# Kernel optimization log

Measured on AMD Instinct MI355X. Metric: run time of the kernel, lower is better.

## Reference

```python
import jax, jax.numpy as jnp
import numpy as np

B, N, D, H = 4, 1024, 1024, 16
HD = D // H  # 64
EPS = 1e-5


def rotate_half(t):
    # unflatten last dim to (..., HD//2, 2), swap-and-negate, flatten back
    t2 = t.reshape(t.shape[:-1] + (HD // 2, 2))
    x1, x2 = t2[..., 0], t2[..., 1]
    return jnp.stack((-x2, x1), axis=-1).reshape(t.shape)


def setup_inputs() -> dict:
    key = jax.random.key(0)
    ks = jax.random.split(key, 12)
    s = 0.02
    return {
        "x": jax.random.normal(ks[0], (B, N, D), jnp.float32),
        "encoding": jax.random.uniform(ks[1], (2, B, 1, N, HD), jnp.float32),
        "Wqkv_w": jax.random.normal(ks[2], (3 * D, D), jnp.float32) * s,
        "Wqkv_b": jnp.zeros((3 * D,), jnp.float32),
        "out_w": jax.random.normal(ks[3], (D, D), jnp.float32) * s,
        "out_b": jnp.zeros((D,), jnp.float32),
        "ffn1_w": jax.random.normal(ks[4], (2 * D, 2 * D), jnp.float32) * s,
        "ffn1_b": jnp.zeros((2 * D,), jnp.float32),
        "ln_g": jnp.ones((2 * D,), jnp.float32),
        "ln_b": jnp.zeros((2 * D,), jnp.float32),
        "ffn2_w": jax.random.normal(ks[5], (D, 2 * D), jnp.float32) * s,
        "ffn2_b": jnp.zeros((D,), jnp.float32),
    }


def reference(x, encoding, Wqkv_w, Wqkv_b, out_w, out_b,
              ffn1_w, ffn1_b, ln_g, ln_b, ffn2_w, ffn2_b):
    b, n, d = x.shape
    # fused QKV projection: [B,N,3D] -> [B,H,N,HD,3]
    qkv = x @ Wqkv_w.T + Wqkv_b
    qkv = qkv.reshape(b, n, H, HD, 3).transpose(0, 2, 1, 3, 4)
    q, k, v = qkv[..., 0], qkv[..., 1], qkv[..., 2]
    # cached rotary embedding: t*cos + rotate_half(t)*sin
    q = q * encoding[0] + rotate_half(q) * encoding[1]
    k = k * encoding[0] + rotate_half(k) * encoding[1]
    # scaled dot-product attention (mask is None in this path)
    scale = HD ** -0.5
    sim = jnp.einsum('bhid,bhjd->bhij', q, k) * scale
    attn = jax.nn.softmax(sim, axis=-1)
    ctx = jnp.einsum('bhij,bhjd->bhid', attn, v)
    ctx = ctx.transpose(0, 2, 1, 3).reshape(b, n, d)
    message = ctx @ out_w.T + out_b
    # FFN on concat([x, message]) with interposed LayerNorm + GELU (exact)
    h = jnp.concatenate([x, message], axis=-1) @ ffn1_w.T + ffn1_b
    mu = h.mean(-1, keepdims=True)
    var = ((h - mu) ** 2).mean(-1, keepdims=True)
    h = (h - mu) * jax.lax.rsqrt(var + EPS) * ln_g + ln_b
    h = jax.nn.gelu(h, approximate=False)
    return x + h @ ffn2_w.T + ffn2_b
```

## Files before the change

### kernel.cpp

```cpp
#include <hip/hip_runtime.h>
#include <hip/hip_bf16.h>
#include <math.h>

#define B_ 4
#define N_ 1024
#define D_ 1024
#define H_ 16
#define HD_ 64
#define M_ (B_*N_)

typedef __hip_bfloat16 bf16;
using floatx4 = __attribute__((ext_vector_type(4))) float;
using shortx8 = __attribute__((ext_vector_type(8))) short;

__device__ __forceinline__ float to_f(bf16 v) { return __bfloat162float(v); }
__device__ __forceinline__ float s2f(short v) {
    unsigned u = ((unsigned)(unsigned short)v) << 16;
    return __builtin_bit_cast(float, u);
}
__device__ __forceinline__ unsigned short bf_bits(float x) {
    bf16 h = __float2bfloat16(x);
    return *reinterpret_cast<unsigned short*>(&h);
}

#define GLOBAL_AS __attribute__((address_space(1)))
#define LDS_AS    __attribute__((address_space(3)))
__device__ __forceinline__ void load_lds16(const void* g, void* l) {
    __builtin_amdgcn_global_load_lds((const GLOBAL_AS unsigned int*)g,
                                     (LDS_AS unsigned int*)l, 16, 0, 0);
}

__device__ __forceinline__ void storec(float* p, float v) { *p = v; }
__device__ __forceinline__ void storec(bf16*  p, float v) { *p = __float2bfloat16(v); }

template<typename TC, bool RESID, bool SPLIT, int BN>
__global__ __launch_bounds__(256)
void mgemm(const bf16* __restrict__ A, int lda,
           const bf16* __restrict__ A2, int lda2, int K1,
           const bf16* __restrict__ W, int ldw,
           const float* __restrict__ bias,
           const float* __restrict__ resid, int ldr,
           TC* __restrict__ C, int ldc,
           int M, int N, int K)
{
    constexpr int NT  = BN / 32;
    constexpr int ASZ = 128 * 32;
    constexpr int BSZ = BN * 32;
    __shared__ short lds[2 * (ASZ + BSZ)];

    int t = threadIdx.x;
    int lane = t & 63, quad = lane >> 4, l15 = lane & 15;
    int wave = t >> 6, wm = wave & 1, wn = wave >> 1;

    int gx = gridDim.x;
    int bid = blockIdx.y * gx + blockIdx.x;
    int seg = bid / (8 * gx);
    int rem = bid - seg * 8 * gx;
    int bx = rem >> 3;
    int by = seg * 8 + (rem & 7);
    int row0 = by * 128, col0 = bx * BN;

    const short* Ag  = (const short*)A;
    const short* A2g = (const short*)A2;
    const short* Wg  = (const short*)W;

    auto stage = [&](int buf, int k0) {
        short* As = lds + buf * (ASZ + BSZ);
        short* Bs = As + ASZ;
        #pragma unroll
        for (int pass = 0; pass < 2; ++pass) {
            int idx = pass * 256 + t;
            int r = idx >> 2, c8 = (idx & 3) << 3;
            int wub = (pass * 256 + (t & 192)) * 8;
            const short* asrc;
            if (SPLIT && k0 >= K1)
                asrc = A2g + (size_t)(row0 + r) * lda2 + (k0 - K1) + c8;
            else
                asrc = Ag + (size_t)(row0 + r) * lda + k0 + c8;
            load_lds16(asrc, &As[wub]);
        }
        #pragma unroll
        for (int pass = 0; pass < BN / 64; ++pass) {
            int idx = pass * 256 + t;
            int r = idx >> 2, c8 = (idx & 3) << 3;
            int wub = (pass * 256 + (t & 192)) * 8;
            load_lds16(Wg + (size_t)(col0 + r) * ldw + k0 + c8, &Bs[wub]);
        }
    };

    floatx4 acc[4][NT];
    #pragma unroll
    for (int mt = 0; mt < 4; ++mt)
        #pragma unroll
        for (int nt = 0; nt < NT; ++nt)
            acc[mt][nt] = (floatx4){0.f, 0.f, 0.f, 0.f};

    stage(0, 0);
    int buf = 0;
    for (int k0 = 0; k0 < K; k0 += 32, buf ^= 1) {
        __syncthreads();
        const short* As = lds + buf * (ASZ + BSZ);
        const short* Bs = As + ASZ;
        shortx8 af[4], bfv[NT];
        #pragma unroll
        for (int mt = 0; mt < 4; ++mt)
            af[mt] = *(const shortx8*)&As[(wm * 64 + mt * 16 + l15) * 32 + quad * 8];
        #pragma unroll
        for (int nt = 0; nt < NT; ++nt)
            bfv[nt] = *(const shortx8*)&Bs[(wn * (BN / 2) + nt * 16 + l15) * 32 + quad * 8];
        if (k0 + 32 < K) stage(buf ^ 1, k0 + 32);
        #pragma unroll
        for (int mt = 0; mt < 4; ++mt)
            #pragma unroll
            for (int nt = 0; nt < NT; ++nt)
                acc[mt][nt] = __builtin_amdgcn_mfma_f32_16x16x32_bf16(
                    af[mt], bfv[nt], acc[mt][nt], 0, 0, 0);
    }

    #pragma unroll
    for (int mt = 0; mt < 4; ++mt) {
        #pragma unroll
        for (int nt = 0; nt < NT; ++nt) {
            int col = col0 + wn * (BN / 2) + nt * 16 + l15;
            float bv = bias[col];
            #pragma unroll
            for (int r = 0; r < 4; ++r) {
                int row = row0 + wm * 64 + mt * 16 + quad * 4 + r;
                float v = acc[mt][nt][r] + bv;
                if (RESID) v += resid[(size_t)row * ldr + col];
                storec(&C[(size_t)row * ldc + col], v);
            }
        }
    }
}

__global__ void f2b_all(const float* __restrict__ s0, bf16* __restrict__ d0,
                        const float* __restrict__ s1, bf16* __restrict__ d1,
                        const float* __restrict__ s2, bf16* __restrict__ d2,
                        const float* __restrict__ s3, bf16* __restrict__ d3,
                        const float* __restrict__ s4, bf16* __restrict__ d4)
{
    int blk = blockIdx.x;
    const float* s; bf16* d; int base;
    if      (blk < 4096)  { s = s0; d = d0; base = blk; }
    else if (blk < 7168)  { s = s1; d = d1; base = blk - 4096; }
    else if (blk < 8192)  { s = s2; d = d2; base = blk - 7168; }
    else if (blk < 12288) { s = s3; d = d3; base = blk - 8192; }
    else                  { s = s4; d = d4; base = blk - 12288; }
    int i = base * 1024 + threadIdx.x * 4;
    float4 v = *(const float4*)&s[i];
    d[i + 0] = __float2bfloat16(v.x);
    d[i + 1] = __float2bfloat16(v.y);
    d[i + 2] = __float2bfloat16(v.z);
    d[i + 3] = __float2bfloat16(v.w);
}

#define RS 196
__global__ __launch_bounds__(256)
void rope_all(const bf16* __restrict__ qkv, const float* __restrict__ enc,
              bf16* __restrict__ q, bf16* __restrict__ k, bf16* __restrict__ vt)
{
    __shared__ short raw[64 * RS];
    int n0 = blockIdx.x * 64, h = blockIdx.y, b = blockIdx.z;
    int t = threadIdx.x;
    const short* qg = (const short*)qkv;

    {
        int row = t >> 2, off = (t & 3) * 48;
        const short* src = qg + ((size_t)(b * N_ + n0 + row)) * 3072 + h * 192 + off;
        uint4 u[3];
        u[0] = ((const uint4*)src)[0];
        u[1] = ((const uint4*)src)[1];
        u[2] = ((const uint4*)src)[2];
        uint4 u2[3];
        u2[0] = ((const uint4*)src)[3];
        u2[1] = ((const uint4*)src)[4];
        u2[2] = ((const uint4*)src)[5];
        uint2* dst = (uint2*)&raw[row * RS + off];
        const uint2* p = (const uint2*)u;
        #pragma unroll
        for (int i = 0; i < 6; ++i) dst[i] = p[i];
        const uint2* p2 = (const uint2*)u2;
        #pragma unroll
        for (int i = 0; i < 6; ++i) dst[6 + i] = p2[i];
    }
    __syncthreads();

    size_t bh = (size_t)(b * H_ + h);
    {
        int d = t & 63, g0 = t >> 6;
        int dp = d ^ 1;
        float sgn = (d & 1) ? 1.0f : -1.0f;
        #pragma unroll
        for (int i = 0; i < 16; ++i) {
            int nl = g0 + 4 * i;
            const short* r = &raw[nl * RS];
            float qv = s2f(r[3 * d]),  kv = s2f(r[3 * d + 1]);
            float qp = s2f(r[3 * dp]), kp = s2f(r[3 * dp + 1]);
            size_t ei = ((size_t)(b * N_ + n0 + nl)) * HD_ + d;
            float c = enc[ei];
            float s = enc[(size_t)B_ * N_ * HD_ + ei];
            size_t o = (bh * N_ + n0 + nl) * HD_ + d;
            q[o] = __float2bfloat16(qv * c + sgn * qp * s);
            k[o] = __float2bfloat16(kv * c + sgn * kp * s);
        }
    }
    {
        int nl = t & 63, g0 = t >> 6;
        #pragma unroll
        for (int i = 0; i < 16; ++i) {
            int dt = g0 + 4 * i;
            vt[(bh * HD_ + dt) * N_ + n0 + nl] =
                *reinterpret_cast<bf16*>(&raw[nl * RS + 3 * dt + 2]);
        }
    }
}

__global__ __launch_bounds__(256, 2)
void fattn(const bf16* __restrict__ q, const bf16* __restrict__ k,
           const bf16* __restrict__ vt, bf16* __restrict__ ctx)
{
    const int i0 = blockIdx.x * 128;
    const int h = blockIdx.y, b = blockIdx.z;
    const int t = threadIdx.x;
    const int lane = t & 63;
    const int w = t >> 6;
    const int quad = lane >> 4, l15 = lane & 15;

    __shared__ alignas(16) short Ks[64 * 72];
    __shared__ alignas(16) short Vs[64 * 72];
    __shared__ alignas(16) short Ps[128 * 72];

    const size_t bh = (size_t)(b * H_ + h) * N_;
    const size_t bhv = (size_t)(b * H_ + h) * HD_;
    const short* qg = (const short*)q;
    const short* kg = (const short*)k;
    const short* vg = (const short*)vt;

    shortx8 qf[2][2];
    #pragma unroll
    for (int rt = 0; rt < 2; ++rt) {
        const short* qrow = qg + (bh + i0 + w * 32 + rt * 16 + l15) * HD_;
        qf[rt][0] = *(const shortx8*)(qrow + quad * 8);
        qf[rt][1] = *(const shortx8*)(qrow + 32 + quad * 8);
    }

    floatx4 O[2][4];
    #pragma unroll
    for (int rt = 0; rt < 2; ++rt)
        #pragma unroll
        for (int dt = 0; dt < 4; ++dt) O[rt][dt] = (floatx4){0.f, 0.f, 0.f, 0.f};
    float lsum[2] = {0.f, 0.f};

    const int srow = t >> 2, soff = (t & 3) * 16;

    for (int j0 = 0; j0 < N_; j0 += 64) {
        __syncthreads();
        {
            const uint4* src = (const uint4*)(kg + (bh + j0 + srow) * HD_ + soff);
            uint4 a0 = src[0], a1 = src[1];
            *(uint4*)&Ks[srow * 72 + soff]     = a0;
            *(uint4*)&Ks[srow * 72 + soff + 8] = a1;
        }
        {
            const uint4* src = (const uint4*)(vg + (bhv + srow) * N_ + j0 + soff);
            uint4 a0 = src[0], a1 = src[1];
            *(uint4*)&Vs[srow * 72 + soff]     = a0;
            *(uint4*)&Vs[srow * 72 + soff + 8] = a1;
        }
        __syncthreads();

        floatx4 ST[4][2];
        #pragma unroll
        for (int kt = 0; kt < 4; ++kt) {
            shortx8 a0 = *(const shortx8*)&Ks[(kt * 16 + l15) * 72 + quad * 8];
            shortx8 a1 = *(const shortx8*)&Ks[(kt * 16 + l15) * 72 + 32 + quad * 8];
            #pragma unroll
            for (int rt = 0; rt < 2; ++rt) {
                floatx4 c = (floatx4){0.f, 0.f, 0.f, 0.f};
                c = __builtin_amdgcn_mfma_f32_16x16x32_bf16(a0, qf[rt][0], c, 0, 0, 0);
                c = __builtin_amdgcn_mfma_f32_16x16x32_bf16(a1, qf[rt][1], c, 0, 0, 0);
                ST[kt][rt] = c;
            }
        }

        #pragma unroll
        for (int kt = 0; kt < 4; ++kt)
            #pragma unroll
            for (int rt = 0; rt < 2; ++rt) {
                unsigned short pk[4];
                #pragma unroll
                for (int r = 0; r < 4; ++r) {
                    float e = __expf(ST[kt][rt][r] * 0.125f);
                    lsum[rt] += e;
                    pk[r] = bf_bits(e);
                }
                *(uint2*)&Ps[(w * 32 + rt * 16 + l15) * 72 + kt * 16 + quad * 4] =
                    *(const uint2*)pk;
            }

        shortx8 pa[2][2];
        #pragma unroll
        for (int rt = 0; rt < 2; ++rt) {
            pa[rt][0] = *(const shortx8*)&Ps[(w * 32 + rt * 16 + l15) * 72 + quad * 8];
            pa[rt][1] = *(const shortx8*)&Ps[(w * 32 + rt * 16 + l15) * 72 + 32 + quad * 8];
        }
        #pragma unroll
        for (int dt = 0; dt < 4; ++dt) {
            shortx8 vb0 = *(const shortx8*)&Vs[(dt * 16 + l15) * 72 + quad * 8];
            shortx8 vb1 = *(const shortx8*)&Vs[(dt * 16 + l15) * 72 + 32 + quad * 8];
            #pragma unroll
            for (int rt = 0; rt < 2; ++rt) {
                O[rt][dt] = __builtin_amdgcn_mfma_f32_16x16x32_bf16(pa[rt][0], vb0, O[rt][dt], 0, 0, 0);
                O[rt][dt] = __builtin_amdgcn_mfma_f32_16x16x32_bf16(pa[rt][1], vb1, O[rt][dt], 0, 0, 0);
            }
        }
    }

    #pragma unroll
    for (int rt = 0; rt < 2; ++rt) {
        float rs = lsum[rt];
        rs += __shfl_xor(rs, 16);
        rs += __shfl_xor(rs, 32);
        #pragma unroll
        for (int r = 0; r < 4; ++r) {
            float inv = 1.0f / __shfl(rs, quad * 4 + r);
            int row = i0 + w * 32 + rt * 16 + quad * 4 + r;
            #pragma unroll
            for (int dt = 0; dt < 4; ++dt)
                ctx[((size_t)(b * N_ + row)) * D_ + h * HD_ + dt * 16 + l15] =
                    __float2bfloat16(O[rt][dt][r] * inv);
        }
    }
}

__global__ void ln_gelu(bf16* __restrict__ hbuf, const float* __restrict__ g,
                        const float* __restrict__ beta)
{
    int row = blockIdx.x;
    int t = threadIdx.x;
    bf16* hr = hbuf + (size_t)row * 2048;
    float vals[8];
    float s = 0.f, s2 = 0.f;
    #pragma unroll
    for (int l = 0; l < 8; ++l) {
        float x = to_f(hr[t + 256 * l]);
        vals[l] = x; s += x; s2 += x * x;
    }
    __shared__ float rs[256], rs2[256];
    rs[t] = s; rs2[t] = s2; __syncthreads();
    for (int k2 = 128; k2 > 0; k2 >>= 1) {
        if (t < k2) { rs[t] += rs[t + k2]; rs2[t] += rs2[t + k2]; }
        __syncthreads();
    }
    float mu  = rs[0] * (1.0f / 2048.0f);
    float var = rs2[0] * (1.0f / 2048.0f) - mu * mu;
    float rstd = rsqrtf(var + 1e-5f);
    #pragma unroll
    for (int l = 0; l < 8; ++l) {
        int c = t + 256 * l;
        float xn = (vals[l] - mu) * rstd * g[c] + beta[c];
        hr[c] = __float2bfloat16(0.5f * xn * (1.0f + erff(xn * 0.70710678118654752f)));
    }
}

extern "C" void kernel_launch(void* const* d_in, const int* in_sizes, int n_in,
                              void* d_out, int out_size, void* d_ws, size_t ws_size,
                              hipStream_t stream)
{
    const float* x      = (const float*)d_in[0];
    const float* enc    = (const float*)d_in[1];
    const float* Wqkv_w = (const float*)d_in[2];
    const float* Wqkv_b = (const float*)d_in[3];
    const float* out_w  = (const float*)d_in[4];
    const float* out_b  = (const float*)d_in[5];
    const float* ffn1_w = (const float*)d_in[6];
    const float* ffn1_b = (const float*)d_in[7];
    const float* ln_g   = (const float*)d_in[8];
    const float* ln_b   = (const float*)d_in[9];
    const float* ffn2_w = (const float*)d_in[10];
    const float* ffn2_b = (const float*)d_in[11];
    float* out = (float*)d_out;

    float* ws = (float*)d_ws;
    bf16* qkv16 = (bf16*)ws;
    bf16* ctx16 = (bf16*)ws;
    bf16* h16   = (bf16*)(ws + 2097152);
    bf16* q16   = (bf16*)(ws + 6291456);
    bf16* k16   = q16 + 2097152;
    bf16* vt16  = k16 + 2097152;
    bf16* msg16 = (bf16*)(ws + 6291456);
    bf16* x16   = (bf16*)(ws + 12582912);
    bf16* wq16  = (bf16*)(ws + 14680064);
    bf16* wo16  = wq16 + 3145728;
    bf16* wf1   = wo16 + 1048576;
    bf16* wf2   = wf1 + 4194304;

    f2b_all<<<14336, 256, 0, stream>>>(x, x16, Wqkv_w, wq16, out_w, wo16,
                                       ffn1_w, wf1, ffn2_w, wf2);

    dim3 g1(3072 / 128, 4096 / 128);
    mgemm<bf16, false, false, 128><<<g1, 256, 0, stream>>>(
        x16, 1024, nullptr, 0, 0, wq16, 1024, Wqkv_b, nullptr, 0,
        qkv16, 3072, 4096, 3072, 1024);

    dim3 gr(16, 16, 4);
    rope_all<<<gr, 256, 0, stream>>>(qkv16, enc, q16, k16, vt16);

    dim3 ga(N_ / 128, H_, B_);
    fattn<<<ga, 256, 0, stream>>>(q16, k16, vt16, ctx16);

    dim3 g2(1024 / 64, 4096 / 128);
    mgemm<bf16, false, false, 64><<<g2, 256, 0, stream>>>(
        ctx16, 1024, nullptr, 0, 0, wo16, 1024, out_b, nullptr, 0,
        msg16, 1024, 4096, 1024, 1024);

    dim3 g3(2048 / 128, 4096 / 128);
    mgemm<bf16, false, true, 128><<<g3, 256, 0, stream>>>(
        x16, 1024, msg16, 1024, 1024, wf1, 2048, ffn1_b, nullptr, 0,
        h16, 2048, 4096, 2048, 2048);

    ln_gelu<<<4096, 256, 0, stream>>>(h16, ln_g, ln_b);

    dim3 g4(1024 / 64, 4096 / 128);
    mgemm<float, true, false, 64><<<g4, 256, 0, stream>>>(
        h16, 2048, nullptr, 0, 0, wf2, 2048, ffn2_b, x, 1024,
        out, 1024, 4096, 1024, 2048);
}
```

Measured before the change: 300.2 us.

## Prefetch attention K/V tiles, remap GEMM blocks across XCDs, vectorize LN-GELU

The attention loop now loads the next K/V tile into registers while computing on the current one, and raises wave priority around the MFMA sections. The GEMM block-index mapping is permuted so consecutive workgroups spread across the eight XCDs. The LN+GELU kernel switches to 128-bit vector loads and stores and a shuffle-based reduction in place of the LDS tree. Together these aim to hide global-load latency, improve L2 locality, and cut synchronisation, at the cost of extra registers for the prefetch.

```diff
diff --git a/kernel.cpp b/kernel.cpp
--- a/kernel.cpp
+++ b/kernel.cpp
@@ -53,7 +53,11 @@
     int wave = t >> 6, wm = wave & 1, wn = wave >> 1;
 
     int gx = gridDim.x;
-    int bid = blockIdx.y * gx + blockIdx.x;
+    int nwg = gx * gridDim.y;
+    int p = blockIdx.y * gx + blockIdx.x;
+    int bid;
+    if (nwg & 7) bid = p;
+    else         bid = (p & 7) * (nwg >> 3) + (p >> 3);
     int seg = bid / (8 * gx);
     int rem = bid - seg * 8 * gx;
     int bx = rem >> 3;
@@ -253,24 +257,34 @@
     float lsum[2] = {0.f, 0.f};
 
     const int srow = t >> 2, soff = (t & 3) * 16;
+    const short* kst = kg + (bh + srow) * HD_ + soff;
+    const short* vst = vg + (bhv + srow) * N_ + soff;
+
+    uint4 ka0, ka1, va0, va1;
+    ka0 = ((const uint4*)kst)[0];
+    ka1 = ((const uint4*)kst)[1];
+    va0 = ((const uint4*)vst)[0];
+    va1 = ((const uint4*)vst)[1];
 
     for (int j0 = 0; j0 < N_; j0 += 64) {
         __syncthreads();
-        {
-            const uint4* src = (const uint4*)(kg + (bh + j0 + srow) * HD_ + soff);
-            uint4 a0 = src[0], a1 = src[1];
-            *(uint4*)&Ks[srow * 72 + soff]     = a0;
-            *(uint4*)&Ks[srow * 72 + soff + 8] = a1;
-        }
-        {
-            const uint4* src = (const uint4*)(vg + (bhv + srow) * N_ + j0 + soff);
-            uint4 a0 = src[0], a1 = src[1];
-            *(uint4*)&Vs[srow * 72 + soff]     = a0;
-            *(uint4*)&Vs[srow * 72 + soff + 8] = a1;
-        }
+        *(uint4*)&Ks[srow * 72 + soff]     = ka0;
+        *(uint4*)&Ks[srow * 72 + soff + 8] = ka1;
+        *(uint4*)&Vs[srow * 72 + soff]     = va0;
+        *(uint4*)&Vs[srow * 72 + soff + 8] = va1;
         __syncthreads();
 
+        if (j0 + 64 < N_) {
+            const short* kn = kst + (size_t)(j0 + 64) * HD_;
+            const short* vn = vst + (j0 + 64);
+            ka0 = ((const uint4*)kn)[0];
+            ka1 = ((const uint4*)kn)[1];
+            va0 = ((const uint4*)vn)[0];
+            va1 = ((const uint4*)vn)[1];
+        }
+
         floatx4 ST[4][2];
+        __builtin_amdgcn_s_setprio(1);
         #pragma unroll
         for (int kt = 0; kt < 4; ++kt) {
             shortx8 a0 = *(const shortx8*)&Ks[(kt * 16 + l15) * 72 + quad * 8];
@@ -283,6 +297,7 @@
                 ST[kt][rt] = c;
             }
         }
+        __builtin_amdgcn_s_setprio(0);
 
         #pragma unroll
         for (int kt = 0; kt < 4; ++kt)
@@ -305,6 +320,7 @@
             pa[rt][0] = *(const shortx8*)&Ps[(w * 32 + rt * 16 + l15) * 72 + quad * 8];
             pa[rt][1] = *(const shortx8*)&Ps[(w * 32 + rt * 16 + l15) * 72 + 32 + quad * 8];
         }
+        __builtin_amdgcn_s_setprio(1);
         #pragma unroll
         for (int dt = 0; dt < 4; ++dt) {
             shortx8 vb0 = *(const shortx8*)&Vs[(dt * 16 + l15) * 72 + quad * 8];
@@ -315,6 +331,7 @@
                 O[rt][dt] = __builtin_amdgcn_mfma_f32_16x16x32_bf16(pa[rt][1], vb1, O[rt][dt], 0, 0, 0);
             }
         }
+        __builtin_amdgcn_s_setprio(0);
     }
 
     #pragma unroll
@@ -339,29 +356,46 @@
 {
     int row = blockIdx.x;
     int t = threadIdx.x;
-    bf16* hr = hbuf + (size_t)row * 2048;
+    short* hr = (short*)hbuf + (size_t)row * 2048;
+
+    shortx8 v = *(const shortx8*)&hr[t * 8];
     float vals[8];
     float s = 0.f, s2 = 0.f;
     #pragma unroll
     for (int l = 0; l < 8; ++l) {
-        float x = to_f(hr[t + 256 * l]);
+        float x = s2f(v[l]);
         vals[l] = x; s += x; s2 += x * x;
     }
-    __shared__ float rs[256], rs2[256];
-    rs[t] = s; rs2[t] = s2; __syncthreads();
-    for (int k2 = 128; k2 > 0; k2 >>= 1) {
-        if (t < k2) { rs[t] += rs[t + k2]; rs2[t] += rs2[t + k2]; }
-        __syncthreads();
-    }
-    float mu  = rs[0] * (1.0f / 2048.0f);
-    float var = rs2[0] * (1.0f / 2048.0f) - mu * mu;
+    #pragma unroll
+    for (int off = 32; off >= 1; off >>= 1) {
+        s  += __shfl_xor(s,  off);
+        s2 += __shfl_xor(s2, off);
+    }
+    __shared__ float ws_[4], ws2_[4];
+    if ((t & 63) == 0) { ws_[t >> 6] = s; ws2_[t >> 6] = s2; }
+    __syncthreads();
+    float S  = ws_[0] + ws_[1] + ws_[2] + ws_[3];
+    float S2 = ws2_[0] + ws2_[1] + ws2_[2] + ws2_[3];
+
+    float mu  = S * (1.0f / 2048.0f);
+    float var = S2 * (1.0f / 2048.0f) - mu * mu;
     float rstd = rsqrtf(var + 1e-5f);
+
+    float4 g0 = *(const float4*)&g[t * 8];
+    float4 g1 = *(const float4*)&g[t * 8 + 4];
+    float4 b0 = *(const float4*)&beta[t * 8];
+    float4 b1 = *(const float4*)&beta[t * 8 + 4];
+    float gv[8] = {g0.x, g0.y, g0.z, g0.w, g1.x, g1.y, g1.z, g1.w};
+    float bv[8] = {b0.x, b0.y, b0.z, b0.w, b1.x, b1.y, b1.z, b1.w};
+
+    shortx8 o;
     #pragma unroll
     for (int l = 0; l < 8; ++l) {
-        int c = t + 256 * l;
-        float xn = (vals[l] - mu) * rstd * g[c] + beta[c];
-        hr[c] = __float2bfloat16(0.5f * xn * (1.0f + erff(xn * 0.70710678118654752f)));
-    }
+        float xn = (vals[l] - mu) * rstd * gv[l] + bv[l];
+        float ge = 0.5f * xn * (1.0f + erff(xn * 0.70710678118654752f));
+        o[l] = (short)bf_bits(ge);
+    }
+    *(shortx8*)&hr[t * 8] = o;
 }
 
 extern "C" void kernel_launch(void* const* d_in, const int* in_sizes, int n_in,
```

Result: faster. 289.5 us (-3.6%).
